# Kernel tuning notes

Hardware: AMD Instinct MI355X
Metric: run time of the kernel (lower is better)

## Reference

```python
import jax, jax.numpy as jnp
import numpy as np

B, L, H = 2, 256, 256
EXPAND = 2
I = H * EXPAND        # internal_size = 512
S = I                 # state_size must equal internal_size (see broadcast in selective mechanism)
K = 3                 # d_conv (must be odd so 'same' padding holds)
EPS = 1e-5


def _forward(x, W_in, conv_w, conv_b, W_ssm, b_ssm, W_gate, b_gate, A, D, W_out, z, ln_g, ln_b):
    # in_proj: [B,L,H] @ [2I,H]^T -> [B,L,2I] (no bias)
    xp = jnp.einsum('blh,oh->blo', x, W_in)
    x_q, x_k = xp[..., :I], xp[..., I:]
    # conv1d over time, full channel mixing (I -> I), 'same' padding, with bias
    xk = jnp.transpose(x_k, (0, 2, 1))  # [B,I,L]
    xk = jax.lax.conv_general_dilated(xk, conv_w, (1,), [((K - 1) // 2, (K - 1) // 2)],
                                      dimension_numbers=('NCH', 'OIH', 'NCH'))
    xk = xk + conv_b[None, :, None]
    x_k = jnp.transpose(xk, (0, 2, 1))  # [B,L,I]
    x_q = jax.nn.gelu(x_q, approximate=False)  # torch F.gelu default = exact erf
    xc = x_q + x_k  # x_combined [B,L,I]

    # selective mechanism
    ssm = jnp.einsum('bli,oi->blo', xc, W_ssm) + b_ssm      # [B,L,2S+I]
    gate = jax.nn.sigmoid(jnp.einsum('bli,oi->blo', xc, W_gate) + b_gate)  # [B,L,S+I]
    C_w = ssm[..., S:2 * S]          # [B,L,S]
    D_w = ssm[..., 2 * S:]           # [B,L,I]
    C_weight = gate[..., S:] * C_w   # requires S == I
    D_weight = D_w * D_w

    x_out = xc * D_weight            # [B,L,I]
    u = x_out[..., :S]               # state input [B,L,S]

    # recurrence: h_0 = u_0 (broadcast over I); h_t = h_{t-1} * A + u_t (broadcast over I)
    # (init h = 0 reproduces the i==0 branch: 0*A + u_0)
    def step(h, u_t):
        h = h * A + u_t[:, :, None]  # [B,S,I]
        return h, h

    h0 = jnp.zeros((B, S, I), x_out.dtype)
    _, hs = jax.lax.scan(step, h0, jnp.transpose(u, (1, 0, 2)))  # hs: [L,B,S,I]

    C_applied = jnp.einsum('lbsi,bls->bli', hs, C_weight)  # [B,L,I]
    y = C_applied + x_out * D
    out = jnp.einsum('bli,hi->blh', y, W_out)  # out_proj, no bias

    # LayerNorm over last dim
    mu = jnp.mean(out, axis=-1, keepdims=True)
    var = jnp.mean(jnp.square(out - mu), axis=-1, keepdims=True)
    out = (out - mu) * jax.lax.rsqrt(var + EPS) * ln_g + ln_b

    out = out * z  # z is shape (1,)
    return out + x


def setup_inputs() -> dict:
    key = jax.random.key(0)
    ks = jax.random.split(key, 10)
    n = lambda k, shape, s: jax.random.normal(k, shape, jnp.float32) * s
    return {
        'x': n(ks[0], (B, L, H), 1.0),
        'W_in': n(ks[1], (2 * I, H), 1.0 / np.sqrt(H)),
        'conv_w': n(ks[2], (I, I, K), 1.0 / np.sqrt(I * K)),
        'conv_b': n(ks[3], (I,), 0.02),
        'W_ssm': n(ks[4], (2 * S + I, I), 1.0 / np.sqrt(I)),
        'b_ssm': n(ks[5], (2 * S + I,), 0.02),
        'W_gate': n(ks[6], (S + I, I), 1.0 / np.sqrt(I)),
        'b_gate': n(ks[7], (S + I,), 0.02),
        'A': jax.random.uniform(ks[8], (S, I), jnp.float32, 0.0, 0.95),  # keep recurrence stable
        'D': jnp.ones((I,), jnp.float32),
        'W_out': n(ks[9], (H, I), 1.0 / np.sqrt(I)),
        'z': jnp.ones((1,), jnp.float32),
        'ln_g': jnp.ones((H,), jnp.float32),
        'ln_b': jnp.zeros((H,), jnp.float32),
    }


def reference(x, W_in, conv_w, conv_b, W_ssm, b_ssm, W_gate, b_gate, A, D, W_out, z, ln_g, ln_b):
    return _forward(x, W_in, conv_w, conv_b, W_ssm, b_ssm, W_gate, b_gate, A, D, W_out, z, ln_g, ln_b)
```

## Files before the change

### kernel.cpp

```cpp
#include <hip/hip_runtime.h>
#include <math.h>

#define NB    2
#define LSEQ  256
#define HDIM  256
#define IDIM  512
#define NROW  512
#define ESZ   1536
#define NC    8
#define TCH   32

typedef __attribute__((ext_vector_type(8))) short bf16x8;
typedef __attribute__((ext_vector_type(4))) float f32x4;

__device__ inline unsigned short f2b(float f) {
    unsigned u = __float_as_uint(f);
    return (unsigned short)((u + 0x7FFFu + ((u >> 16) & 1u)) >> 16);
}

__global__ __launch_bounds__(256) void kcvt(const float* __restrict__ x,
                                            const float* __restrict__ W_in,
                                            const float* __restrict__ conv_w,
                                            const float* __restrict__ W_ssm,
                                            const float* __restrict__ W_gate,
                                            const float* __restrict__ b_ssm,
                                            const float* __restrict__ b_gate,
                                            const float* __restrict__ W_out,
                                            unsigned short* __restrict__ xb,
                                            unsigned short* __restrict__ Wb,
                                            unsigned short* __restrict__ cwb,
                                            unsigned short* __restrict__ Wsgb,
                                            float* __restrict__ bsg,
                                            unsigned short* __restrict__ W_outb) {
    const int stride = gridDim.x * 256;
    const int t0 = blockIdx.x * 256 + threadIdx.x;
    for (int i = t0; i < 131072; i += stride) xb[i] = f2b(x[i]);
    for (int i = t0; i < 262144; i += stride) Wb[i] = f2b(W_in[i]);
    for (int d = t0; d < 262144; d += stride) {
        const float* s = conv_w + (size_t)d * 3;
        cwb[d]          = f2b(s[0]);
        cwb[262144 + d] = f2b(s[1]);
        cwb[524288 + d] = f2b(s[2]);
    }
    for (int d = t0; d < 786432; d += stride) {
        int j = d >> 9, i = d & 511;
        float v = (j < 1024) ? W_ssm[(size_t)(512 + j) * 512 + i]
                             : W_gate[(size_t)(j - 512) * 512 + i];
        Wsgb[d] = f2b(v);
    }
    for (int j = t0; j < 1536; j += stride)
        bsg[j] = (j < 1024) ? b_ssm[512 + j] : b_gate[j - 512];
    for (int i = t0; i < 131072; i += stride) W_outb[i] = f2b(W_out[i]);
}

__global__ __launch_bounds__(256) void k1_mfma(const unsigned short* __restrict__ xb,
                                               const unsigned short* __restrict__ Wb,
                                               float* __restrict__ xq_g,
                                               unsigned short* __restrict__ xkb) {
    const int t = threadIdx.x;
    const int w = blockIdx.x * 4 + (t >> 6);
    const int lane = t & 63;
    const int mt = w >> 6, nt = w & 63;
    const int r0 = mt * 16, n0 = nt * 16;
    const int fr = lane & 15, fk = (lane >> 4) * 8;
    const unsigned short* ap = xb + (size_t)(r0 + fr) * HDIM + fk;
    const unsigned short* bp = Wb + (size_t)(n0 + fr) * HDIM + fk;
    f32x4 acc = {0.f, 0.f, 0.f, 0.f};
    #pragma unroll
    for (int k0 = 0; k0 < HDIM; k0 += 32) {
        bf16x8 av = *(const bf16x8*)(ap + k0);
        bf16x8 bv = *(const bf16x8*)(bp + k0);
        acc = __builtin_amdgcn_mfma_f32_16x16x32_bf16(av, bv, acc, 0, 0, 0);
    }
    const int orow = (lane >> 4) * 4;
    const int oc = n0 + fr;
    if (oc < IDIM) {
        #pragma unroll
        for (int j = 0; j < 4; ++j) {
            float v = acc[j];
            xq_g[(size_t)(r0 + orow + j) * IDIM + oc] =
                0.5f * v * (1.0f + erff(v * 0.70710678118654752f));
        }
    } else {
        #pragma unroll
        for (int j = 0; j < 4; ++j)
            xkb[(size_t)(r0 + orow + j) * IDIM + (oc - IDIM)] = f2b(acc[j]);
    }
}

__global__ __launch_bounds__(256) void kxc_mfma(const unsigned short* __restrict__ xkb,
                                                const unsigned short* __restrict__ cwb,
                                                const float* __restrict__ xq_g,
                                                const float* __restrict__ conv_b,
                                                float* __restrict__ xc,
                                                unsigned short* __restrict__ xcb) {
    const int t = threadIdx.x;
    const int w = blockIdx.x * 4 + (t >> 6);
    const int lane = t & 63;
    const int mt = w >> 5, nt = w & 31;
    const int r0 = mt * 16, o0 = nt * 16;
    const int fr = lane & 15, fk = (lane >> 4) * 8;
    const int g = r0 + fr;
    const int lo = r0 & ~255, hi = lo + 256;
    const bool okm = (g - 1 >= lo), okp = (g + 1 < hi);
    const unsigned short* am = xkb + (size_t)(g - 1) * IDIM + fk;
    const unsigned short* a0 = xkb + (size_t)g * IDIM + fk;
    const unsigned short* ap = xkb + (size_t)(g + 1) * IDIM + fk;
    const unsigned short* b0 = cwb + (size_t)(o0 + fr) * IDIM + fk;
    const unsigned short* b1 = b0 + 262144;
    const unsigned short* b2 = b0 + 524288;
    const bf16x8 zz = {0, 0, 0, 0, 0, 0, 0, 0};
    f32x4 acc = {0.f, 0.f, 0.f, 0.f};
    #pragma unroll
    for (int k0 = 0; k0 < IDIM; k0 += 32) {
        bf16x8 avm = okm ? *(const bf16x8*)(am + k0) : zz;
        bf16x8 av0 = *(const bf16x8*)(a0 + k0);
        bf16x8 avp = okp ? *(const bf16x8*)(ap + k0) : zz;
        bf16x8 bv0 = *(const bf16x8*)(b0 + k0);
        bf16x8 bv1 = *(const bf16x8*)(b1 + k0);
        bf16x8 bv2 = *(const bf16x8*)(b2 + k0);
        acc = __builtin_amdgcn_mfma_f32_16x16x32_bf16(avm, bv0, acc, 0, 0, 0);
        acc = __builtin_amdgcn_mfma_f32_16x16x32_bf16(av0, bv1, acc, 0, 0, 0);
        acc = __builtin_amdgcn_mfma_f32_16x16x32_bf16(avp, bv2, acc, 0, 0, 0);
    }
    const int orow = (lane >> 4) * 4;
    const int oc = o0 + fr;
    const float cb = conv_b[oc];
    #pragma unroll
    for (int j = 0; j < 4; ++j) {
        int r = r0 + orow + j;
        float v = acc[j] + xq_g[(size_t)r * IDIM + oc] + cb;
        xc[(size_t)r * IDIM + oc] = v;
        xcb[(size_t)r * IDIM + oc] = f2b(v);
    }
}

__global__ __launch_bounds__(256) void k3_mfma(const unsigned short* __restrict__ xcb,
                                               const unsigned short* __restrict__ Wsgb,
                                               const float* __restrict__ bsg,
                                               float* __restrict__ E) {
    const int t = threadIdx.x;
    const int w = blockIdx.x * 4 + (t >> 6);
    const int lane = t & 63;
    const int mt = w / 96, nt = w % 96;
    const int r0 = mt * 16, j0 = nt * 16;
    const int fr = lane & 15, fk = (lane >> 4) * 8;
    const unsigned short* ap = xcb + (size_t)(r0 + fr) * IDIM + fk;
    const unsigned short* bp = Wsgb + (size_t)(j0 + fr) * IDIM + fk;
    f32x4 acc = {0.f, 0.f, 0.f, 0.f};
    #pragma unroll
    for (int k0 = 0; k0 < IDIM; k0 += 32) {
        bf16x8 av = *(const bf16x8*)(ap + k0);
        bf16x8 bv = *(const bf16x8*)(bp + k0);
        acc = __builtin_amdgcn_mfma_f32_16x16x32_bf16(av, bv, acc, 0, 0, 0);
    }
    const int orow = (lane >> 4) * 4;
    const int jc = j0 + fr;
    const float bias = bsg[jc];
    #pragma unroll
    for (int j = 0; j < 4; ++j)
        E[(size_t)(r0 + orow + j) * ESZ + jc] = acc[j] + bias;
}

__global__ __launch_bounds__(256) void k3b_elem(const float* __restrict__ E,
                                                const float* __restrict__ xc,
                                                float* __restrict__ Cw,
                                                float* __restrict__ u) {
    int idx4 = (blockIdx.x * 256 + threadIdx.x) * 4;
    int r = idx4 >> 9, s = idx4 & 511;
    const float* Er = E + (size_t)r * ESZ;
    float4 craw = *(const float4*)&Er[s];
    float4 dw   = *(const float4*)&Er[512 + s];
    float4 graw = *(const float4*)&Er[1024 + s];
    float4 xcv  = *(const float4*)&xc[idx4];
    float4 cw, uv;
    cw.x = craw.x / (1.0f + expf(-graw.x));
    cw.y = craw.y / (1.0f + expf(-graw.y));
    cw.z = craw.z / (1.0f + expf(-graw.z));
    cw.w = craw.w / (1.0f + expf(-graw.w));
    uv.x = xcv.x * dw.x * dw.x;
    uv.y = xcv.y * dw.y * dw.y;
    uv.z = xcv.z * dw.z * dw.z;
    uv.w = xcv.w * dw.w * dw.w;
    *(float4*)&Cw[idx4] = cw;
    *(float4*)&u[idx4]  = uv;
}

__global__ __launch_bounds__(256) void k4a_pass1(const float* __restrict__ u,
                                                 const float* __restrict__ A,
                                                 float* __restrict__ C_loc) {
    const int wave = (blockIdx.x * 256 + threadIdx.x) >> 6;
    const int lane = threadIdx.x & 63;
    const int ig = wave & 127;
    const int c  = (wave >> 7) & (NC - 1);
    const int b  = wave >> 10;
    const int i4 = ig * 4;
    const int s8 = lane * 8;
    float a[8][4], h[8][4];
    #pragma unroll
    for (int j = 0; j < 8; ++j) {
        float4 av = *(const float4*)&A[(size_t)(s8 + j) * IDIM + i4];
        a[j][0] = av.x; a[j][1] = av.y; a[j][2] = av.z; a[j][3] = av.w;
        h[j][0] = 0.f; h[j][1] = 0.f; h[j][2] = 0.f; h[j][3] = 0.f;
    }
    const float* ub = u + ((size_t)b * LSEQ + c * TCH) * IDIM;
    for (int l = 0; l < TCH; ++l) {
        float4 u0 = *(const float4*)(ub + l * IDIM + s8);
        float4 u1 = *(const float4*)(ub + l * IDIM + s8 + 4);
        float uu[8] = {u0.x, u0.y, u0.z, u0.w, u1.x, u1.y, u1.z, u1.w};
        #pragma unroll
        for (int ii = 0; ii < 4; ++ii)
            #pragma unroll
            for (int j = 0; j < 8; ++j)
                h[j][ii] = h[j][ii] * a[j][ii] + uu[j];
    }
    #pragma unroll
    for (int ii = 0; ii < 4; ++ii) {
        float* cp = C_loc + (((size_t)b * NC + c) * IDIM + i4 + ii) * IDIM + s8;
        float4 v0, v1;
        v0.x = h[0][ii]; v0.y = h[1][ii]; v0.z = h[2][ii]; v0.w = h[3][ii];
        v1.x = h[4][ii]; v1.y = h[5][ii]; v1.z = h[6][ii]; v1.w = h[7][ii];
        *(float4*)cp = v0;
        *(float4*)(cp + 4) = v1;
    }
}

__global__ __launch_bounds__(256) void k4b_combine(const float* __restrict__ A,
                                                   float* __restrict__ C_loc) {
    int idx = blockIdx.x * 256 + threadIdx.x;
    int s4 = (idx & 127) * 4;
    int i  = (idx >> 7) & 511;
    int b  = idx >> 16;
    float da[4], h4[4] = {0.0f, 0.0f, 0.0f, 0.0f};
    #pragma unroll
    for (int j = 0; j < 4; ++j) {
        float aa = A[(size_t)(s4 + j) * IDIM + i];
        aa = aa * aa; aa = aa * aa; aa = aa * aa;
        aa = aa * aa; aa = aa * aa;
        da[j] = aa;
    }
    for (int c = 0; c < NC; ++c) {
        size_t base = (((size_t)b * NC + c) * IDIM + i) * IDIM + s4;
        float4 cl = *(const float4*)&C_loc[base];
        float4 hv;
        hv.x = h4[0]; hv.y = h4[1]; hv.z = h4[2]; hv.w = h4[3];
        *(float4*)&C_loc[base] = hv;
        h4[0] = h4[0] * da[0] + cl.x;
        h4[1] = h4[1] * da[1] + cl.y;
        h4[2] = h4[2] * da[2] + cl.z;
        h4[3] = h4[3] * da[3] + cl.w;
    }
}

__global__ __launch_bounds__(256) void k4c_pass2(const float* __restrict__ u,
                                                 const float* __restrict__ Cw,
                                                 const float* __restrict__ A,
                                                 const float* __restrict__ D,
                                                 const float* __restrict__ H,
                                                 unsigned short* __restrict__ ybb) {
    const int wave = (blockIdx.x * 256 + threadIdx.x) >> 6;
    const int lane = threadIdx.x & 63;
    const int ig = wave & 127;
    const int c  = (wave >> 7) & (NC - 1);
    const int b  = wave >> 10;
    const int i4 = ig * 4;
    const int s8 = lane * 8;
    float a[8][4], h[8][4];
    #pragma unroll
    for (int j = 0; j < 8; ++j) {
        float4 av = *(const float4*)&A[(size_t)(s8 + j) * IDIM + i4];
        a[j][0] = av.x; a[j][1] = av.y; a[j][2] = av.z; a[j][3] = av.w;
    }
    #pragma unroll
    for (int ii = 0; ii < 4; ++ii) {
        const float* hp = H + (((size_t)b * NC + c) * IDIM + i4 + ii) * IDIM + s8;
        float4 h0v = *(const float4*)hp;
        float4 h1v = *(const float4*)(hp + 4);
        h[0][ii] = h0v.x; h[1][ii] = h0v.y; h[2][ii] = h0v.z; h[3][ii] = h0v.w;
        h[4][ii] = h1v.x; h[5][ii] = h1v.y; h[6][ii] = h1v.z; h[7][ii] = h1v.w;
    }
    float4 Dv = *(const float4*)&D[i4];
    const float Di[4] = {Dv.x, Dv.y, Dv.z, Dv.w};
    const float* ub = u + (size_t)b * LSEQ * IDIM;
    const float* cb = Cw + (size_t)b * LSEQ * IDIM;
    unsigned short* yb = ybb + (size_t)b * LSEQ * IDIM;
    for (int l0 = c * TCH; l0 < c * TCH + TCH; l0 += 4) {
        float p[4][4];
        #pragma unroll
        for (int j = 0; j < 4; ++j) {
            const int l = l0 + j;
            float4 u0 = *(const float4*)(ub + l * IDIM + s8);
            float4 u1 = *(const float4*)(ub + l * IDIM + s8 + 4);
            float4 c0 = *(const float4*)(cb + l * IDIM + s8);
            float4 c1 = *(const float4*)(cb + l * IDIM + s8 + 4);
            float uu[8] = {u0.x, u0.y, u0.z, u0.w, u1.x, u1.y, u1.z, u1.w};
            float cc[8] = {c0.x, c0.y, c0.z, c0.w, c1.x, c1.y, c1.z, c1.w};
            #pragma unroll
            for (int ii = 0; ii < 4; ++ii) {
                float acc = 0.f;
                #pragma unroll
                for (int k = 0; k < 8; ++k) {
                    h[k][ii] = h[k][ii] * a[k][ii] + uu[k];
                    acc += cc[k] * h[k][ii];
                }
                p[j][ii] = acc;
            }
        }
        #pragma unroll
        for (int off = 1; off < 64; off <<= 1) {
            #pragma unroll
            for (int j = 0; j < 4; ++j)
                #pragma unroll
                for (int ii = 0; ii < 4; ++ii)
                    p[j][ii] += __shfl_xor(p[j][ii], off, 64);
        }
        if (lane == 0) {
            #pragma unroll
            for (int j = 0; j < 4; ++j) {
                float4 uli = *(const float4*)&ub[(size_t)(l0 + j) * IDIM + i4];
                const float ul[4] = {uli.x, uli.y, uli.z, uli.w};
                #pragma unroll
                for (int ii = 0; ii < 4; ++ii)
                    yb[(size_t)(l0 + j) * IDIM + i4 + ii] = f2b(p[j][ii] + ul[ii] * Di[ii]);
            }
        }
    }
}

__global__ __launch_bounds__(256) void k5a_mfma(const unsigned short* __restrict__ ybb,
                                                const unsigned short* __restrict__ W_outb,
                                                float* __restrict__ outlin) {
    const int t = threadIdx.x;
    const int w = blockIdx.x * 4 + (t >> 6);
    const int lane = t & 63;
    const int mt = w >> 4, nt = w & 15;
    const int r0 = mt * 16, h0 = nt * 16;
    const int fr = lane & 15, fk = (lane >> 4) * 8;
    const unsigned short* ap = ybb + (size_t)(r0 + fr) * IDIM + fk;
    const unsigned short* bp = W_outb + (size_t)(h0 + fr) * IDIM + fk;
    f32x4 acc = {0.f, 0.f, 0.f, 0.f};
    #pragma unroll
    for (int k0 = 0; k0 < IDIM; k0 += 32) {
        bf16x8 av = *(const bf16x8*)(ap + k0);
        bf16x8 bv = *(const bf16x8*)(bp + k0);
        acc = __builtin_amdgcn_mfma_f32_16x16x32_bf16(av, bv, acc, 0, 0, 0);
    }
    const int orow = (lane >> 4) * 4;
    const int hc = h0 + fr;
    #pragma unroll
    for (int j = 0; j < 4; ++j)
        outlin[(size_t)(r0 + orow + j) * HDIM + hc] = acc[j];
}

__global__ __launch_bounds__(256) void k5b_ln(const float* __restrict__ outlin,
                                              const float* __restrict__ x,
                                              const float* __restrict__ z,
                                              const float* __restrict__ ln_g,
                                              const float* __restrict__ ln_b,
                                              float* __restrict__ out) {
    const int r = blockIdx.x;
    const int t = threadIdx.x;
    float v = outlin[(size_t)r * HDIM + t];
    float s1 = v, s2 = v * v;
    #pragma unroll
    for (int off = 1; off < 64; off <<= 1) {
        s1 += __shfl_xor(s1, off, 64);
        s2 += __shfl_xor(s2, off, 64);
    }
    __shared__ float r1[4], r2[4];
    const int w = t >> 6, lane = t & 63;
    if (lane == 0) { r1[w] = s1; r2[w] = s2; }
    __syncthreads();
    float t1 = r1[0] + r1[1] + r1[2] + r1[3];
    float t2 = r2[0] + r2[1] + r2[2] + r2[3];
    float mu = t1 * (1.0f / 256.0f);
    float var = t2 * (1.0f / 256.0f) - mu * mu;
    float inv = rsqrtf(var + 1e-5f);
    float o = (v - mu) * inv * ln_g[t] + ln_b[t];
    out[(size_t)r * HDIM + t] = o * z[0] + x[(size_t)r * HDIM + t];
}

extern "C" void kernel_launch(void* const* d_in, const int* in_sizes, int n_in,
                              void* d_out, int out_size, void* d_ws, size_t ws_size,
                              hipStream_t stream) {
    const float* x      = (const float*)d_in[0];
    const float* W_in   = (const float*)d_in[1];
    const float* conv_w = (const float*)d_in[2];
    const float* conv_b = (const float*)d_in[3];
    const float* W_ssm  = (const float*)d_in[4];
    const float* b_ssm  = (const float*)d_in[5];
    const float* W_gate = (const float*)d_in[6];
    const float* b_gate = (const float*)d_in[7];
    const float* A      = (const float*)d_in[8];
    const float* D      = (const float*)d_in[9];
    const float* W_out  = (const float*)d_in[10];
    const float* z      = (const float*)d_in[11];
    const float* ln_g   = (const float*)d_in[12];
    const float* ln_b   = (const float*)d_in[13];
    float* out = (float*)d_out;

    float* ws = (float*)d_ws;
    float*          xq_g   = ws;
    float*          xc     = ws + 262144;
    float*          E      = ws + 524288;
    float*          Cw     = ws + 1310720;
    float*          u      = ws + 1572864;
    float*          outlin = ws + 1835008;
    float*          bsg    = ws + 1966080;
    unsigned short* xcb    = (unsigned short*)(ws + 1968128);
    unsigned short* xkb    = (unsigned short*)(ws + 2099200);
    unsigned short* Wsgb   = (unsigned short*)(ws + 2230272);
    unsigned short* W_outb = (unsigned short*)(ws + 2623488);
    unsigned short* ybb    = (unsigned short*)(ws + 2689024);
    float*          area   = ws + 2820096;
    unsigned short* xb     = (unsigned short*)area;
    unsigned short* Wb     = (unsigned short*)(area + 65536);
    unsigned short* cwb    = (unsigned short*)(area + 196608);
    float*          C_loc  = area;

    kcvt      <<<512, 256, 0, stream>>>(x, W_in, conv_w, W_ssm, W_gate, b_ssm,
                                        b_gate, W_out, xb, Wb, cwb, Wsgb, bsg, W_outb);
    k1_mfma   <<<512, 256, 0, stream>>>(xb, Wb, xq_g, xkb);
    kxc_mfma  <<<256, 256, 0, stream>>>(xkb, cwb, xq_g, conv_b, xc, xcb);
    k3_mfma   <<<768, 256, 0, stream>>>(xcb, Wsgb, bsg, E);
    k3b_elem  <<<256, 256, 0, stream>>>(E, xc, Cw, u);
    k4a_pass1 <<<512, 256, 0, stream>>>(u, A, C_loc);
    k4b_combine<<<512, 256, 0, stream>>>(A, C_loc);
    k4c_pass2 <<<512, 256, 0, stream>>>(u, Cw, A, D, C_loc, ybb);
    k5a_mfma  <<<128, 256, 0, stream>>>(ybb, W_outb, outlin);
    k5b_ln    <<<512, 256, 0, stream>>>(outlin, x, z, ln_g, ln_b, out);
}
```

Measured before the change: 104.2 us.

## Fuse selective GEMM with gating epilogue and widen scan tiles to 8 columns

The separate selective-projection GEMM and its elementwise sigmoid/square kernel are merged. Each wave now computes the C, D and gate tiles for the same 16 columns and applies the epilogue directly, so the 1536-wide E intermediate is no longer written and re-read. Separately, the two chunked-scan passes now process 8 internal columns per wave instead of 4. This halves the wave count and reuses each u/Cw load across more columns, at the cost of roughly doubled register pressure (64-element a/h arrays) and lower occupancy.

```diff
diff --git a/kernel.cpp b/kernel.cpp
--- a/kernel.cpp
+++ b/kernel.cpp
@@ -6,7 +6,6 @@
 #define HDIM  256
 #define IDIM  512
 #define NROW  512
-#define ESZ   1536
 #define NC    8
 #define TCH   32
 
@@ -135,55 +134,49 @@
     }
 }
 
-__global__ __launch_bounds__(256) void k3_mfma(const unsigned short* __restrict__ xcb,
-                                               const unsigned short* __restrict__ Wsgb,
-                                               const float* __restrict__ bsg,
-                                               float* __restrict__ E) {
+__global__ __launch_bounds__(256) void k3f_mfma(const unsigned short* __restrict__ xcb,
+                                                const unsigned short* __restrict__ Wsgb,
+                                                const float* __restrict__ bsg,
+                                                const float* __restrict__ xc,
+                                                float* __restrict__ Cw,
+                                                float* __restrict__ u) {
     const int t = threadIdx.x;
     const int w = blockIdx.x * 4 + (t >> 6);
     const int lane = t & 63;
-    const int mt = w / 96, nt = w % 96;
-    const int r0 = mt * 16, j0 = nt * 16;
+    const int mt = w >> 5, nt = w & 31;
+    const int r0 = mt * 16, s0 = nt * 16;
     const int fr = lane & 15, fk = (lane >> 4) * 8;
     const unsigned short* ap = xcb + (size_t)(r0 + fr) * IDIM + fk;
-    const unsigned short* bp = Wsgb + (size_t)(j0 + fr) * IDIM + fk;
-    f32x4 acc = {0.f, 0.f, 0.f, 0.f};
+    const unsigned short* b0 = Wsgb + (size_t)(s0 + fr) * IDIM + fk;
+    const unsigned short* b1 = Wsgb + (size_t)(512 + s0 + fr) * IDIM + fk;
+    const unsigned short* b2 = Wsgb + (size_t)(1024 + s0 + fr) * IDIM + fk;
+    f32x4 ac0 = {0.f, 0.f, 0.f, 0.f};
+    f32x4 ac1 = {0.f, 0.f, 0.f, 0.f};
+    f32x4 ac2 = {0.f, 0.f, 0.f, 0.f};
     #pragma unroll
     for (int k0 = 0; k0 < IDIM; k0 += 32) {
-        bf16x8 av = *(const bf16x8*)(ap + k0);
-        bf16x8 bv = *(const bf16x8*)(bp + k0);
-        acc = __builtin_amdgcn_mfma_f32_16x16x32_bf16(av, bv, acc, 0, 0, 0);
+        bf16x8 av  = *(const bf16x8*)(ap + k0);
+        bf16x8 bv0 = *(const bf16x8*)(b0 + k0);
+        bf16x8 bv1 = *(const bf16x8*)(b1 + k0);
+        bf16x8 bv2 = *(const bf16x8*)(b2 + k0);
+        ac0 = __builtin_amdgcn_mfma_f32_16x16x32_bf16(av, bv0, ac0, 0, 0, 0);
+        ac1 = __builtin_amdgcn_mfma_f32_16x16x32_bf16(av, bv1, ac1, 0, 0, 0);
+        ac2 = __builtin_amdgcn_mfma_f32_16x16x32_bf16(av, bv2, ac2, 0, 0, 0);
     }
     const int orow = (lane >> 4) * 4;
-    const int jc = j0 + fr;
-    const float bias = bsg[jc];
-    #pragma unroll
-    for (int j = 0; j < 4; ++j)
-        E[(size_t)(r0 + orow + j) * ESZ + jc] = acc[j] + bias;
-}
-
-__global__ __launch_bounds__(256) void k3b_elem(const float* __restrict__ E,
-                                                const float* __restrict__ xc,
-                                                float* __restrict__ Cw,
-                                                float* __restrict__ u) {
-    int idx4 = (blockIdx.x * 256 + threadIdx.x) * 4;
-    int r = idx4 >> 9, s = idx4 & 511;
-    const float* Er = E + (size_t)r * ESZ;
-    float4 craw = *(const float4*)&Er[s];
-    float4 dw   = *(const float4*)&Er[512 + s];
-    float4 graw = *(const float4*)&Er[1024 + s];
-    float4 xcv  = *(const float4*)&xc[idx4];
-    float4 cw, uv;
-    cw.x = craw.x / (1.0f + expf(-graw.x));
-    cw.y = craw.y / (1.0f + expf(-graw.y));
-    cw.z = craw.z / (1.0f + expf(-graw.z));
-    cw.w = craw.w / (1.0f + expf(-graw.w));
-    uv.x = xcv.x * dw.x * dw.x;
-    uv.y = xcv.y * dw.y * dw.y;
-    uv.z = xcv.z * dw.z * dw.z;
-    uv.w = xcv.w * dw.w * dw.w;
-    *(float4*)&Cw[idx4] = cw;
-    *(float4*)&u[idx4]  = uv;
+    const int sc = s0 + fr;
+    const float bc = bsg[sc], bd = bsg[512 + sc], bg = bsg[1024 + sc];
+    #pragma unroll
+    for (int j = 0; j < 4; ++j) {
+        int r = r0 + orow + j;
+        float craw = ac0[j] + bc;
+        float dw   = ac1[j] + bd;
+        float graw = ac2[j] + bg;
+        float gv = 1.0f / (1.0f + expf(-graw));
+        float xcv = xc[(size_t)r * IDIM + sc];
+        Cw[(size_t)r * IDIM + sc] = gv * craw;
+        u[(size_t)r * IDIM + sc]  = xcv * dw * dw;
+    }
 }
 
 __global__ __launch_bounds__(256) void k4a_pass1(const float* __restrict__ u,
@@ -191,17 +184,20 @@
                                                  float* __restrict__ C_loc) {
     const int wave = (blockIdx.x * 256 + threadIdx.x) >> 6;
     const int lane = threadIdx.x & 63;
-    const int ig = wave & 127;
-    const int c  = (wave >> 7) & (NC - 1);
-    const int b  = wave >> 10;
-    const int i4 = ig * 4;
+    const int ig = wave & 63;
+    const int c  = (wave >> 6) & (NC - 1);
+    const int b  = wave >> 9;
+    const int i8 = ig * 8;
     const int s8 = lane * 8;
-    float a[8][4], h[8][4];
+    float a[8][8], h[8][8];
     #pragma unroll
     for (int j = 0; j < 8; ++j) {
-        float4 av = *(const float4*)&A[(size_t)(s8 + j) * IDIM + i4];
-        a[j][0] = av.x; a[j][1] = av.y; a[j][2] = av.z; a[j][3] = av.w;
-        h[j][0] = 0.f; h[j][1] = 0.f; h[j][2] = 0.f; h[j][3] = 0.f;
+        float4 a0 = *(const float4*)&A[(size_t)(s8 + j) * IDIM + i8];
+        float4 a1 = *(const float4*)&A[(size_t)(s8 + j) * IDIM + i8 + 4];
+        a[j][0] = a0.x; a[j][1] = a0.y; a[j][2] = a0.z; a[j][3] = a0.w;
+        a[j][4] = a1.x; a[j][5] = a1.y; a[j][6] = a1.z; a[j][7] = a1.w;
+        #pragma unroll
+        for (int ii = 0; ii < 8; ++ii) h[j][ii] = 0.f;
     }
     const float* ub = u + ((size_t)b * LSEQ + c * TCH) * IDIM;
     for (int l = 0; l < TCH; ++l) {
@@ -209,14 +205,14 @@
         float4 u1 = *(const float4*)(ub + l * IDIM + s8 + 4);
         float uu[8] = {u0.x, u0.y, u0.z, u0.w, u1.x, u1.y, u1.z, u1.w};
         #pragma unroll
-        for (int ii = 0; ii < 4; ++ii)
+        for (int ii = 0; ii < 8; ++ii)
             #pragma unroll
             for (int j = 0; j < 8; ++j)
                 h[j][ii] = h[j][ii] * a[j][ii] + uu[j];
     }
     #pragma unroll
-    for (int ii = 0; ii < 4; ++ii) {
-        float* cp = C_loc + (((size_t)b * NC + c) * IDIM + i4 + ii) * IDIM + s8;
+    for (int ii = 0; ii < 8; ++ii) {
+        float* cp = C_loc + (((size_t)b * NC + c) * IDIM + i8 + ii) * IDIM + s8;
         float4 v0, v1;
         v0.x = h[0][ii]; v0.y = h[1][ii]; v0.z = h[2][ii]; v0.w = h[3][ii];
         v1.x = h[4][ii]; v1.y = h[5][ii]; v1.z = h[6][ii]; v1.w = h[7][ii];
@@ -260,34 +256,37 @@
                                                  unsigned short* __restrict__ ybb) {
     const int wave = (blockIdx.x * 256 + threadIdx.x) >> 6;
     const int lane = threadIdx.x & 63;
-    const int ig = wave & 127;
-    const int c  = (wave >> 7) & (NC - 1);
-    const int b  = wave >> 10;
-    const int i4 = ig * 4;
+    const int ig = wave & 63;
+    const int c  = (wave >> 6) & (NC - 1);
+    const int b  = wave >> 9;
+    const int i8 = ig * 8;
     const int s8 = lane * 8;
-    float a[8][4], h[8][4];
+    float a[8][8], h[8][8];
     #pragma unroll
     for (int j = 0; j < 8; ++j) {
-        float4 av = *(const float4*)&A[(size_t)(s8 + j) * IDIM + i4];
-        a[j][0] = av.x; a[j][1] = av.y; a[j][2] = av.z; a[j][3] = av.w;
-    }
-    #pragma unroll
-    for (int ii = 0; ii < 4; ++ii) {
-        const float* hp = H + (((size_t)b * NC + c) * IDIM + i4 + ii) * IDIM + s8;
+        float4 a0 = *(const float4*)&A[(size_t)(s8 + j) * IDIM + i8];
+        float4 a1 = *(const float4*)&A[(size_t)(s8 + j) * IDIM + i8 + 4];
+        a[j][0] = a0.x; a[j][1] = a0.y; a[j][2] = a0.z; a[j][3] = a0.w;
+        a[j][4] = a1.x; a[j][5] = a1.y; a[j][6] = a1.z; a[j][7] = a1.w;
+    }
+    #pragma unroll
+    for (int ii = 0; ii < 8; ++ii) {
+        const float* hp = H + (((size_t)b * NC + c) * IDIM + i8 + ii) * IDIM + s8;
         float4 h0v = *(const float4*)hp;
         float4 h1v = *(const float4*)(hp + 4);
         h[0][ii] = h0v.x; h[1][ii] = h0v.y; h[2][ii] = h0v.z; h[3][ii] = h0v.w;
         h[4][ii] = h1v.x; h[5][ii] = h1v.y; h[6][ii] = h1v.z; h[7][ii] = h1v.w;
     }
-    float4 Dv = *(const float4*)&D[i4];
-    const float Di[4] = {Dv.x, Dv.y, Dv.z, Dv.w};
+    float4 D0 = *(const float4*)&D[i8];
+    float4 D1 = *(const float4*)&D[i8 + 4];
+    const float Di[8] = {D0.x, D0.y, D0.z, D0.w, D1.x, D1.y, D1.z, D1.w};
     const float* ub = u + (size_t)b * LSEQ * IDIM;
     const float* cb = Cw + (size_t)b * LSEQ * IDIM;
     unsigned short* yb = ybb + (size_t)b * LSEQ * IDIM;
-    for (int l0 = c * TCH; l0 < c * TCH + TCH; l0 += 4) {
-        float p[4][4];
-        #pragma unroll
-        for (int j = 0; j < 4; ++j) {
+    for (int l0 = c * TCH; l0 < c * TCH + TCH; l0 += 2) {
+        float p[2][8];
+        #pragma unroll
+        for (int j = 0; j < 2; ++j) {
             const int l = l0 + j;
             float4 u0 = *(const float4*)(ub + l * IDIM + s8);
             float4 u1 = *(const float4*)(ub + l * IDIM + s8 + 4);
@@ -296,7 +295,7 @@
             float uu[8] = {u0.x, u0.y, u0.z, u0.w, u1.x, u1.y, u1.z, u1.w};
             float cc[8] = {c0.x, c0.y, c0.z, c0.w, c1.x, c1.y, c1.z, c1.w};
             #pragma unroll
-            for (int ii = 0; ii < 4; ++ii) {
+            for (int ii = 0; ii < 8; ++ii) {
                 float acc = 0.f;
                 #pragma unroll
                 for (int k = 0; k < 8; ++k) {
@@ -309,19 +308,21 @@
         #pragma unroll
         for (int off = 1; off < 64; off <<= 1) {
             #pragma unroll
-            for (int j = 0; j < 4; ++j)
+            for (int j = 0; j < 2; ++j)
                 #pragma unroll
-                for (int ii = 0; ii < 4; ++ii)
+                for (int ii = 0; ii < 8; ++ii)
                     p[j][ii] += __shfl_xor(p[j][ii], off, 64);
         }
         if (lane == 0) {
             #pragma unroll
-            for (int j = 0; j < 4; ++j) {
-                float4 uli = *(const float4*)&ub[(size_t)(l0 + j) * IDIM + i4];
-                const float ul[4] = {uli.x, uli.y, uli.z, uli.w};
+            for (int j = 0; j < 2; ++j) {
+                float4 ul0 = *(const float4*)&ub[(size_t)(l0 + j) * IDIM + i8];
+                float4 ul1 = *(const float4*)&ub[(size_t)(l0 + j) * IDIM + i8 + 4];
+                const float ul[8] = {ul0.x, ul0.y, ul0.z, ul0.w,
+                                     ul1.x, ul1.y, ul1.z, ul1.w};
                 #pragma unroll
-                for (int ii = 0; ii < 4; ++ii)
-                    yb[(size_t)(l0 + j) * IDIM + i4 + ii] = f2b(p[j][ii] + ul[ii] * Di[ii]);
+                for (int ii = 0; ii < 8; ++ii)
+                    yb[(size_t)(l0 + j) * IDIM + i8 + ii] = f2b(p[j][ii] + ul[ii] * Di[ii]);
             }
         }
     }
@@ -402,31 +403,29 @@
     float* ws = (float*)d_ws;
     float*          xq_g   = ws;
     float*          xc     = ws + 262144;
-    float*          E      = ws + 524288;
-    float*          Cw     = ws + 1310720;
-    float*          u      = ws + 1572864;
-    float*          outlin = ws + 1835008;
-    float*          bsg    = ws + 1966080;
-    unsigned short* xcb    = (unsigned short*)(ws + 1968128);
-    unsigned short* xkb    = (unsigned short*)(ws + 2099200);
-    unsigned short* Wsgb   = (unsigned short*)(ws + 2230272);
-    unsigned short* W_outb = (unsigned short*)(ws + 2623488);
-    unsigned short* ybb    = (unsigned short*)(ws + 2689024);
-    float*          area   = ws + 2820096;
+    float*          Cw     = ws + 524288;
+    float*          u      = ws + 786432;
+    float*          outlin = ws + 1048576;
+    float*          bsg    = ws + 1179648;
+    unsigned short* xcb    = (unsigned short*)(ws + 1181696);
+    unsigned short* xkb    = (unsigned short*)(ws + 1312768);
+    unsigned short* Wsgb   = (unsigned short*)(ws + 1443840);
+    unsigned short* W_outb = (unsigned short*)(ws + 1837056);
+    unsigned short* ybb    = (unsigned short*)(ws + 1902592);
+    float*          area   = ws + 2033664;
     unsigned short* xb     = (unsigned short*)area;
     unsigned short* Wb     = (unsigned short*)(area + 65536);
     unsigned short* cwb    = (unsigned short*)(area + 196608);
     float*          C_loc  = area;
 
-    kcvt      <<<512, 256, 0, stream>>>(x, W_in, conv_w, W_ssm, W_gate, b_ssm,
-                                        b_gate, W_out, xb, Wb, cwb, Wsgb, bsg, W_outb);
-    k1_mfma   <<<512, 256, 0, stream>>>(xb, Wb, xq_g, xkb);
-    kxc_mfma  <<<256, 256, 0, stream>>>(xkb, cwb, xq_g, conv_b, xc, xcb);
-    k3_mfma   <<<768, 256, 0, stream>>>(xcb, Wsgb, bsg, E);
-    k3b_elem  <<<256, 256, 0, stream>>>(E, xc, Cw, u);
-    k4a_pass1 <<<512, 256, 0, stream>>>(u, A, C_loc);
+    kcvt       <<<512, 256, 0, stream>>>(x, W_in, conv_w, W_ssm, W_gate, b_ssm,
+                                         b_gate, W_out, xb, Wb, cwb, Wsgb, bsg, W_outb);
+    k1_mfma    <<<512, 256, 0, stream>>>(xb, Wb, xq_g, xkb);
+    kxc_mfma   <<<256, 256, 0, stream>>>(xkb, cwb, xq_g, conv_b, xc, xcb);
+    k3f_mfma   <<<256, 256, 0, stream>>>(xcb, Wsgb, bsg, xc, Cw, u);
+    k4a_pass1  <<<256, 256, 0, stream>>>(u, A, C_loc);
     k4b_combine<<<512, 256, 0, stream>>>(A, C_loc);
-    k4c_pass2 <<<512, 256, 0, stream>>>(u, Cw, A, D, C_loc, ybb);
-    k5a_mfma  <<<128, 256, 0, stream>>>(ybb, W_outb, outlin);
-    k5b_ln    <<<512, 256, 0, stream>>>(outlin, x, z, ln_g, ln_b, out);
-}
+    k4c_pass2  <<<256, 256, 0, stream>>>(u, Cw, A, D, C_loc, ybb);
+    k5a_mfma   <<<128, 256, 0, stream>>>(ybb, W_outb, outlin);
+    k5b_ln     <<<512, 256, 0, stream>>>(outlin, x, z, ln_g, ln_b, out);
+}
```

Measured after the change: 103.2 us. About the same (-0.9%).
